# Kernel tuning notes

Measured on AMD Instinct MI355X. Metric: run time of the kernel, lower is better.

The kernel has to match this reference:

```python
import jax, jax.numpy as jnp
import numpy as np

RADIUS = 0.1
NSAMPLE = 32
B, N, NPOINT, C = 4, 8192, 2048, 64


def ball_query(xyz, new_xyz, fps_idx):
    """Faithful to pointnet2 ball_query CUDA kernel: for each centroid collect up to
    NSAMPLE in-radius point indices in scan order; slots beyond the count are padded
    with the first in-radius index (0 if the ball is empty). fps_idx is prepended."""
    n = xyz.shape[1]
    # squared distances (B, npoint, N)
    d2 = jnp.sum((new_xyz[:, :, None, :] - xyz[:, None, :, :]) ** 2, axis=-1)
    valid = d2 < jnp.float32(RADIUS) ** 2
    cand = jnp.where(valid, jnp.arange(n, dtype=jnp.int32), jnp.int32(n))
    cand = jnp.sort(cand, axis=-1)[:, :, :NSAMPLE]  # first NSAMPLE valid ids, N = sentinel
    first = cand[:, :, :1]
    pad = jnp.where(first < n, first, 0)            # pad with first valid (0 if none)
    idx = jnp.where(cand < n, cand, pad)
    return jnp.concatenate([fps_idx[:, :, None], idx], axis=2)  # (B, npoint, NSAMPLE+1)


def group(features, idx):
    # features (B, C, N), idx (B, npoint, K) -> (B, C, npoint, K)
    return jax.vmap(lambda f, i: f[:, i])(features, idx)


def setup_inputs() -> dict:
    key = jax.random.key(0)
    k1, k2, k3 = jax.random.split(key, 3)
    xyz = jax.random.uniform(k1, (B, N, 3), dtype=jnp.float32)
    fps_idx = jax.random.randint(k2, (B, NPOINT), 0, N, dtype=jnp.int32)
    new_xyz = jax.vmap(lambda p, i: p[i])(xyz, fps_idx)  # centroids are real points
    features = jax.random.normal(k3, (B, C, N), dtype=jnp.float32)
    return {"xyz": xyz, "new_xyz": new_xyz, "features": features, "fps_idx": fps_idx}


def reference(xyz, new_xyz, features, fps_idx):
    idx = jax.lax.stop_gradient(ball_query(xyz, new_xyz, fps_idx))
    grouped_xyz = group(jnp.swapaxes(xyz, 1, 2), idx)              # (B, 3, npoint, K)
    centered = grouped_xyz - jnp.swapaxes(new_xyz, 1, 2)[..., None]
    # NOTE: the torch module uses in-place `grouped_xyz -= ...`, so raw_grouped_xyz
    # aliases the centered tensor -> both concat slots hold centered coordinates.
    grouped_features = group(features, idx)                        # (B, C, npoint, K)
    return jnp.concatenate([centered, centered, grouped_features], axis=1)
```

## Files before the change

kernel.cpp:

```cpp
#include <hip/hip_runtime.h>
#include <stdint.h>
#include <limits.h>

constexpr int BB      = 4;
constexpr int NN      = 8192;
constexpr int NPOINT  = 2048;
constexpr int CC      = 64;
constexpr int NSAMPLE = 32;
constexpr int KTOT    = NSAMPLE + 1;
constexpr int NCH     = 3 + 3 + CC;
constexpr int CHS     = NPOINT * KTOT;

constexpr int   GG     = 5;
constexpr int   NCELL  = GG * GG * GG;
constexpr float RPADF  = 0.1001f;
constexpr int   CAND_CAP = 192;

__device__ __forceinline__ int cell_of(float x, float y, float z) {
    int ix = (int)floorf(x * 5.0f); ix = ix < 0 ? 0 : (ix > 4 ? 4 : ix);
    int iy = (int)floorf(y * 5.0f); iy = iy < 0 ? 0 : (iy > 4 ? 4 : iy);
    int iz = (int)floorf(z * 5.0f); iz = iz < 0 ? 0 : (iz > 4 ? 4 : iz);
    return (ix * GG + iy) * GG + iz;
}

__global__ __launch_bounds__(1024) void grid_build(
    const float* __restrict__ xyz, int* __restrict__ cellstartg,
    float4* __restrict__ spt)
{
    __shared__ int hist[NCELL];
    __shared__ int csl[NCELL + 1];
    __shared__ int cur[NCELL];
    const int b = blockIdx.x;
    const int t = threadIdx.x;
    if (t < NCELL) hist[t] = 0;
    __syncthreads();
    const float* xb = xyz + (size_t)b * NN * 3;
    float px[NN / 1024], py[NN / 1024], pz[NN / 1024];
    int   pc[NN / 1024];
#pragma unroll
    for (int k = 0; k < NN / 1024; ++k) {
        const float* p = xb + (size_t)(t + k * 1024) * 3;
        px[k] = p[0]; py[k] = p[1]; pz[k] = p[2];
        pc[k] = cell_of(px[k], py[k], pz[k]);
        atomicAdd(&hist[pc[k]], 1);
    }
    __syncthreads();
    if (t < 64) {
        int x0 = hist[t];
        int x1 = (t + 64 < NCELL) ? hist[t + 64] : 0;
#pragma unroll
        for (int d = 1; d < 64; d <<= 1) {
            int t0 = __shfl_up(x0, d);
            int t1 = __shfl_up(x1, d);
            if (t >= d) { x0 += t0; x1 += t1; }
        }
        x1 += __shfl(x0, 63);
        if (t == 0) csl[0] = 0;
        csl[1 + t] = x0;
        if (t <= 60) csl[65 + t] = x1;
    }
    __syncthreads();
    if (t < NCELL + 1) cellstartg[b * (NCELL + 1) + t] = csl[t];
    if (t < NCELL)     cur[t] = csl[t];
    __syncthreads();
#pragma unroll
    for (int k = 0; k < NN / 1024; ++k) {
        const int pos = atomicAdd(&cur[pc[k]], 1);
        spt[b * NN + pos] = make_float4(px[k], py[k], pz[k],
                                        __int_as_float(t + k * 1024));
    }
}

__global__ __launch_bounds__(256) void ball_query_grid(
    const float4* __restrict__ spt, const int* __restrict__ cellstart,
    const float* __restrict__ new_xyz, const int* __restrict__ fps_idx,
    int*         __restrict__ idx_out)
{
    __shared__ int cand[4][CAND_CAP];
    const int w    = threadIdx.x >> 6;
    const int lane = threadIdx.x & 63;
    const int wave = blockIdx.x * 4 + w;
    const int b    = wave >> 11;

    const float* cp = new_xyz + (size_t)wave * 3;
    const float cx = cp[0], cy = cp[1], cz = cp[2];
    const float r2 = __fmul_rn(0.1f, 0.1f);

    int ix0 = (int)floorf((cx - RPADF) * 5.0f); ix0 = ix0 < 0 ? 0 : ix0;
    int ix1 = (int)floorf((cx + RPADF) * 5.0f); ix1 = ix1 > 4 ? 4 : ix1;
    int iy0 = (int)floorf((cy - RPADF) * 5.0f); iy0 = iy0 < 0 ? 0 : iy0;
    int iy1 = (int)floorf((cy + RPADF) * 5.0f); iy1 = iy1 > 4 ? 4 : iy1;
    int iz0 = (int)floorf((cz - RPADF) * 5.0f); iz0 = iz0 < 0 ? 0 : iz0;
    int iz1 = (int)floorf((cz + RPADF) * 5.0f); iz1 = iz1 > 4 ? 4 : iz1;

    const int* cs = cellstart + b * (NCELL + 1);
    const int gb  = b * NN;
    int cnt = 0;

    for (int ix = ix0; ix <= ix1; ++ix) {
        for (int iy = iy0; iy <= iy1; ++iy) {
            const int cbase = (ix * GG + iy) * GG;
            const int st = cs[cbase + iz0];
            const int en = cs[cbase + iz1 + 1];
            for (int base = st; base < en; base += 64) {
                const int pos = base + lane;
                const bool inb = pos < en;
                const float4 q = spt[gb + (inb ? pos : st)];
                const int oid = __float_as_int(q.w);
                const float dx = __fsub_rn(cx, q.x);
                const float dy = __fsub_rn(cy, q.y);
                const float dz = __fsub_rn(cz, q.z);
                const float d2 = __fadd_rn(__fadd_rn(__fmul_rn(dx, dx), __fmul_rn(dy, dy)),
                                           __fmul_rn(dz, dz));
                const bool valid = inb && (d2 < r2);
                const unsigned long long m = __ballot(valid);
                if (m != 0ull) {
                    const int prefix = __builtin_amdgcn_mbcnt_hi(
                        (unsigned)(m >> 32), __builtin_amdgcn_mbcnt_lo((unsigned)m, 0u));
                    const int slot = cnt + prefix;
                    if (valid && slot < CAND_CAP) cand[w][slot] = oid;
                    cnt += (int)__popcll(m);
                }
            }
        }
    }

    const int K = cnt > CAND_CAP ? CAND_CAP : cnt;

    int v0 = (lane       < K) ? cand[w][lane]       : INT_MAX;
    int v1 = (lane + 64  < K) ? cand[w][lane + 64]  : INT_MAX;
    int v2 = (lane + 128 < K) ? cand[w][lane + 128] : INT_MAX;
    int rk0 = 0, rk1 = 0, rk2 = 0;
    for (int j = 0; j < K; ++j) {
        const int sv = cand[w][j];
        rk0 += (sv < v0); rk1 += (sv < v1); rk2 += (sv < v2);
    }
    int* out = idx_out + (size_t)wave * KTOT;
    if (lane       < K && rk0 < NSAMPLE) out[1 + rk0] = v0;
    if (lane + 64  < K && rk1 < NSAMPLE) out[1 + rk1] = v1;
    if (lane + 128 < K && rk2 < NSAMPLE) out[1 + rk2] = v2;

    if (K < NSAMPLE) {
        int mn = v0;
#pragma unroll
        for (int off = 32; off >= 1; off >>= 1) {
            const int o = __shfl_xor(mn, off);
            mn = o < mn ? o : mn;
        }
        const int pad = (K > 0) ? mn : 0;
        if (lane >= K && lane < NSAMPLE) out[1 + lane] = pad;
    }
    if (lane == 0) out[0] = fps_idx[wave];
}

__global__ __launch_bounds__(256) void feat_transpose(
    const float* __restrict__ f, float* __restrict__ ft)
{
    __shared__ float tile[64 * 65];
    const int blk = blockIdx.x;
    const int b   = blk >> 7;
    const int n0  = (blk & 127) << 6;
    const int w   = threadIdx.x >> 6, l = threadIdx.x & 63;
#pragma unroll
    for (int i = 0; i < 16; ++i) {
        const int c = i * 4 + w;
        tile[l * 65 + c] = f[((size_t)b * CC + c) * NN + n0 + l];
    }
    __syncthreads();
#pragma unroll
    for (int i = 0; i < 16; ++i) {
        const int flat = i * 256 + threadIdx.x;
        ft[((size_t)b * NN + n0) * CC + flat] = tile[(flat >> 6) * 65 + (flat & 63)];
    }
}

constexpr int TPAD = 66;
__global__ __launch_bounds__(256) void gather_v7(
    const float* __restrict__ xyz, const float* __restrict__ new_xyz,
    const float4* __restrict__ ft4, const int* __restrict__ idx,
    float* __restrict__ out)
{
    __shared__ float tile[NCH][TPAD];
    const int blk = blockIdx.x;
    const int t   = threadIdx.x;
    const int jj0 = blk * 64;
    const int b   = jj0 / CHS;
    const int jjb = jj0 - b * CHS;

    if (t < 64) {
        const int id = idx[jj0 + t];
        const int j  = (jjb + t) / KTOT;
        const float* gp = xyz + (size_t)(b * NN + id) * 3;
        const float* cp = new_xyz + (size_t)(b * NPOINT + j) * 3;
        const float vx = __fsub_rn(gp[0], cp[0]);
        const float vy = __fsub_rn(gp[1], cp[1]);
        const float vz = __fsub_rn(gp[2], cp[2]);
        tile[0][t] = vx; tile[1][t] = vy; tile[2][t] = vz;
        tile[3][t] = vx; tile[4][t] = vy; tile[5][t] = vz;
    }

    {
        const int r = t >> 2, g = t & 3;
        const int id = idx[jj0 + r];
        const float4* row = ft4 + ((size_t)b * NN + id) * (CC / 4);
        float4 v[4];
#pragma unroll
        for (int i = 0; i < 4; ++i) v[i] = row[4 * i + g];
#pragma unroll
        for (int i = 0; i < 4; ++i) {
            const int c0 = 6 + 16 * i + 4 * g;
            tile[c0 + 0][r] = v[i].x;
            tile[c0 + 1][r] = v[i].y;
            tile[c0 + 2][r] = v[i].z;
            tile[c0 + 3][r] = v[i].w;
        }
    }
    __syncthreads();

    const int w   = t >> 6;
    const int col = t & 63;
    const size_t ob = (size_t)b * NCH * CHS + (size_t)jjb + col;
#pragma unroll
    for (int k = 0; k < 18; ++k) {
        const int ch = 4 * k + w;
        if (ch < NCH) out[ob + (size_t)ch * CHS] = tile[ch][col];
    }
}

__global__ __launch_bounds__(256) void ball_query_bf(
    const float* __restrict__ xyz, const float* __restrict__ new_xyz,
    const int* __restrict__ fps_idx, int* __restrict__ idx_out)
{
    const int wave = (blockIdx.x * blockDim.x + threadIdx.x) >> 6;
    const int lane = threadIdx.x & 63;
    if (wave >= BB * NPOINT) return;
    const int b = wave >> 11;
    const float* cp = new_xyz + (size_t)wave * 3;
    const float cx = cp[0], cy = cp[1], cz = cp[2];
    const float r2 = __fmul_rn(0.1f, 0.1f);
    const float* xb = xyz + (size_t)b * NN * 3;
    int* out = idx_out + (size_t)wave * KTOT;
    int count = 0, first = 0;
    for (int base = 0; base < NN; base += 64) {
        const int p = base + lane;
        const float dx = __fsub_rn(cx, xb[p * 3 + 0]);
        const float dy = __fsub_rn(cy, xb[p * 3 + 1]);
        const float dz = __fsub_rn(cz, xb[p * 3 + 2]);
        const float d2 = __fadd_rn(__fadd_rn(__fmul_rn(dx, dx), __fmul_rn(dy, dy)),
                                   __fmul_rn(dz, dz));
        const bool valid = d2 < r2;
        const unsigned long long m = __ballot(valid);
        if (count == 0 && m != 0ull) first = base + __builtin_ctzll(m);
        const int prefix = __builtin_amdgcn_mbcnt_hi(
            (unsigned)(m >> 32), __builtin_amdgcn_mbcnt_lo((unsigned)m, 0u));
        const int slot = count + prefix;
        if (valid && slot < NSAMPLE) out[1 + slot] = p;
        count += (int)__popcll(m);
        if (count >= NSAMPLE) break;
    }
    if (count < NSAMPLE) {
        const int pad = (count > 0) ? first : 0;
        if (lane >= count && lane < NSAMPLE) out[1 + lane] = pad;
    }
    if (lane == 0) out[0] = fps_idx[wave];
}

__global__ __launch_bounds__(256) void gather_kernel(
    const float* __restrict__ xyz, const float* __restrict__ new_xyz,
    const float* __restrict__ features, const int* __restrict__ idx,
    float* __restrict__ out)
{
    const long long total = (long long)BB * NCH * CHS;
    const long long o = (long long)blockIdx.x * blockDim.x + threadIdx.x;
    if (o >= total) return;
    const int s  = (int)(o % KTOT);
    long long t  = o / KTOT;
    const int j  = (int)(t % NPOINT);
    t /= NPOINT;
    const int ch = (int)(t % NCH);
    const int b  = (int)(t / NCH);
    const int id = idx[(long long)(b * NPOINT + j) * KTOT + s];
    float v;
    if (ch < 6) {
        const int c3 = (ch >= 3) ? (ch - 3) : ch;
        v = __fsub_rn(xyz[((long long)b * NN + id) * 3 + c3],
                      new_xyz[((long long)b * NPOINT + j) * 3 + c3]);
    } else {
        v = features[((long long)b * CC + (ch - 6)) * NN + id];
    }
    out[o] = v;
}

extern "C" void kernel_launch(void* const* d_in, const int* in_sizes, int n_in,
                              void* d_out, int out_size, void* d_ws, size_t ws_size,
                              hipStream_t stream) {
    const float* xyz      = (const float*)d_in[0];
    const float* new_xyz  = (const float*)d_in[1];
    const float* features = (const float*)d_in[2];
    const int*   fps_idx  = (const int*)d_in[3];
    float*       out      = (float*)d_out;

    const size_t off_idx  = 0;
    const size_t sz_idx   = (size_t)BB * CHS * 4;
    const size_t off_ft   = off_idx + sz_idx;
    const size_t sz_ft    = (size_t)BB * NN * CC * 4;
    const size_t off_spt  = off_ft + sz_ft;
    const size_t sz_spt   = (size_t)BB * NN * 16;
    const size_t off_cs   = off_spt + sz_spt;
    const size_t need_full = off_cs + 2048;

    int* idxbuf = (int*)((char*)d_ws + off_idx);

    if (ws_size >= need_full) {
        float*  ft  = (float*) ((char*)d_ws + off_ft);
        float4* spt = (float4*)((char*)d_ws + off_spt);
        int*    cs  = (int*)   ((char*)d_ws + off_cs);

        grid_build<<<BB, 1024, 0, stream>>>(xyz, cs, spt);

        ball_query_grid<<<BB * NPOINT / 4, 256, 0, stream>>>(
            spt, cs, new_xyz, fps_idx, idxbuf);

        feat_transpose<<<BB * (NN / 64), 256, 0, stream>>>(features, ft);
        gather_v7<<<BB * CHS / 64, 256, 0, stream>>>(xyz, new_xyz, (const float4*)ft,
                                                     idxbuf, out);
    } else if (ws_size >= sz_idx) {
        ball_query_bf<<<BB * NPOINT / 4, 256, 0, stream>>>(xyz, new_xyz, fps_idx, idxbuf);
        const long long total = (long long)BB * NCH * CHS;
        gather_kernel<<<(int)((total + 255) / 256), 256, 0, stream>>>(
            xyz, new_xyz, features, idxbuf, out);
    }
}
```

Before: 124.1 us.

## Sort centroids by grid cell for locality and unroll ball-query scan by two

Result: no change. 126.5 us (+1.9%).

```diff
diff --git a/kernel.cpp b/kernel.cpp
--- a/kernel.cpp
+++ b/kernel.cpp
@@ -24,14 +24,16 @@
 }
 
 __global__ __launch_bounds__(1024) void grid_build(
-    const float* __restrict__ xyz, int* __restrict__ cellstartg,
-    float4* __restrict__ spt)
+    const float* __restrict__ xyz, const float* __restrict__ new_xyz,
+    int* __restrict__ cellstartg, float4* __restrict__ spt,
+    int* __restrict__ csortg)
 {
     __shared__ int hist[NCELL];
     __shared__ int csl[NCELL + 1];
     __shared__ int cur[NCELL];
     const int b = blockIdx.x;
     const int t = threadIdx.x;
+
     if (t < NCELL) hist[t] = 0;
     __syncthreads();
     const float* xb = xyz + (size_t)b * NN * 3;
@@ -69,20 +71,57 @@
         spt[b * NN + pos] = make_float4(px[k], py[k], pz[k],
                                         __int_as_float(t + k * 1024));
     }
+
+    __syncthreads();
+    if (t < NCELL) hist[t] = 0;
+    __syncthreads();
+    const float* nb = new_xyz + (size_t)b * NPOINT * 3;
+    int cc[NPOINT / 1024];
+#pragma unroll
+    for (int k = 0; k < NPOINT / 1024; ++k) {
+        const float* p = nb + (size_t)(t + k * 1024) * 3;
+        cc[k] = cell_of(p[0], p[1], p[2]);
+        atomicAdd(&hist[cc[k]], 1);
+    }
+    __syncthreads();
+    if (t < 64) {
+        int x0 = hist[t];
+        int x1 = (t + 64 < NCELL) ? hist[t + 64] : 0;
+#pragma unroll
+        for (int d = 1; d < 64; d <<= 1) {
+            int t0 = __shfl_up(x0, d);
+            int t1 = __shfl_up(x1, d);
+            if (t >= d) { x0 += t0; x1 += t1; }
+        }
+        x1 += __shfl(x0, 63);
+        if (t == 0) csl[0] = 0;
+        csl[1 + t] = x0;
+        if (t <= 60) csl[65 + t] = x1;
+    }
+    __syncthreads();
+    if (t < NCELL) cur[t] = csl[t];
+    __syncthreads();
+#pragma unroll
+    for (int k = 0; k < NPOINT / 1024; ++k) {
+        const int pos = atomicAdd(&cur[cc[k]], 1);
+        csortg[b * NPOINT + pos] = t + k * 1024;
+    }
 }
 
 __global__ __launch_bounds__(256) void ball_query_grid(
     const float4* __restrict__ spt, const int* __restrict__ cellstart,
+    const int* __restrict__ csort,
     const float* __restrict__ new_xyz, const int* __restrict__ fps_idx,
     int*         __restrict__ idx_out)
 {
     __shared__ int cand[4][CAND_CAP];
     const int w    = threadIdx.x >> 6;
     const int lane = threadIdx.x & 63;
-    const int wave = blockIdx.x * 4 + w;
-    const int b    = wave >> 11;
-
-    const float* cp = new_xyz + (size_t)wave * 3;
+    const int sp   = blockIdx.x * 4 + w;
+    const int b    = sp >> 11;
+    const int gc   = b * NPOINT + csort[sp];
+
+    const float* cp = new_xyz + (size_t)gc * 3;
     const float cx = cp[0], cy = cp[1], cz = cp[2];
     const float r2 = __fmul_rn(0.1f, 0.1f);
 
@@ -102,24 +141,44 @@
             const int cbase = (ix * GG + iy) * GG;
             const int st = cs[cbase + iz0];
             const int en = cs[cbase + iz1 + 1];
-            for (int base = st; base < en; base += 64) {
-                const int pos = base + lane;
-                const bool inb = pos < en;
-                const float4 q = spt[gb + (inb ? pos : st)];
-                const int oid = __float_as_int(q.w);
-                const float dx = __fsub_rn(cx, q.x);
-                const float dy = __fsub_rn(cy, q.y);
-                const float dz = __fsub_rn(cz, q.z);
-                const float d2 = __fadd_rn(__fadd_rn(__fmul_rn(dx, dx), __fmul_rn(dy, dy)),
-                                           __fmul_rn(dz, dz));
-                const bool valid = inb && (d2 < r2);
-                const unsigned long long m = __ballot(valid);
-                if (m != 0ull) {
-                    const int prefix = __builtin_amdgcn_mbcnt_hi(
-                        (unsigned)(m >> 32), __builtin_amdgcn_mbcnt_lo((unsigned)m, 0u));
-                    const int slot = cnt + prefix;
-                    if (valid && slot < CAND_CAP) cand[w][slot] = oid;
-                    cnt += (int)__popcll(m);
+            for (int base = st; base < en; base += 128) {
+                const int p0 = base + lane;
+                const int p1 = base + 64 + lane;
+                const bool i0 = p0 < en;
+                const bool i1 = p1 < en;
+                const float4 q0 = spt[gb + (i0 ? p0 : st)];
+                const float4 q1 = spt[gb + (i1 ? p1 : st)];
+                {
+                    const float dx = __fsub_rn(cx, q0.x);
+                    const float dy = __fsub_rn(cy, q0.y);
+                    const float dz = __fsub_rn(cz, q0.z);
+                    const float d2 = __fadd_rn(__fadd_rn(__fmul_rn(dx, dx), __fmul_rn(dy, dy)),
+                                               __fmul_rn(dz, dz));
+                    const bool valid = i0 && (d2 < r2);
+                    const unsigned long long m = __ballot(valid);
+                    if (m != 0ull) {
+                        const int prefix = __builtin_amdgcn_mbcnt_hi(
+                            (unsigned)(m >> 32), __builtin_amdgcn_mbcnt_lo((unsigned)m, 0u));
+                        const int slot = cnt + prefix;
+                        if (valid && slot < CAND_CAP) cand[w][slot] = __float_as_int(q0.w);
+                        cnt += (int)__popcll(m);
+                    }
+                }
+                {
+                    const float dx = __fsub_rn(cx, q1.x);
+                    const float dy = __fsub_rn(cy, q1.y);
+                    const float dz = __fsub_rn(cz, q1.z);
+                    const float d2 = __fadd_rn(__fadd_rn(__fmul_rn(dx, dx), __fmul_rn(dy, dy)),
+                                               __fmul_rn(dz, dz));
+                    const bool valid = i1 && (d2 < r2);
+                    const unsigned long long m = __ballot(valid);
+                    if (m != 0ull) {
+                        const int prefix = __builtin_amdgcn_mbcnt_hi(
+                            (unsigned)(m >> 32), __builtin_amdgcn_mbcnt_lo((unsigned)m, 0u));
+                        const int slot = cnt + prefix;
+                        if (valid && slot < CAND_CAP) cand[w][slot] = __float_as_int(q1.w);
+                        cnt += (int)__popcll(m);
+                    }
                 }
             }
         }
@@ -135,7 +194,7 @@
         const int sv = cand[w][j];
         rk0 += (sv < v0); rk1 += (sv < v1); rk2 += (sv < v2);
     }
-    int* out = idx_out + (size_t)wave * KTOT;
+    int* out = idx_out + (size_t)gc * KTOT;
     if (lane       < K && rk0 < NSAMPLE) out[1 + rk0] = v0;
     if (lane + 64  < K && rk1 < NSAMPLE) out[1 + rk1] = v1;
     if (lane + 128 < K && rk2 < NSAMPLE) out[1 + rk2] = v2;
@@ -150,7 +209,7 @@
         const int pad = (K > 0) ? mn : 0;
         if (lane >= K && lane < NSAMPLE) out[1 + lane] = pad;
     }
-    if (lane == 0) out[0] = fps_idx[wave];
+    if (lane == 0) out[0] = fps_idx[gc];
 }
 
 __global__ __launch_bounds__(256) void feat_transpose(
@@ -307,19 +366,22 @@
     const size_t off_spt  = off_ft + sz_ft;
     const size_t sz_spt   = (size_t)BB * NN * 16;
     const size_t off_cs   = off_spt + sz_spt;
-    const size_t need_full = off_cs + 2048;
+    const size_t off_csort = off_cs + 2048;
+    const size_t sz_csort  = (size_t)BB * NPOINT * 4;
+    const size_t need_full = off_csort + sz_csort;
 
     int* idxbuf = (int*)((char*)d_ws + off_idx);
 
     if (ws_size >= need_full) {
-        float*  ft  = (float*) ((char*)d_ws + off_ft);
-        float4* spt = (float4*)((char*)d_ws + off_spt);
-        int*    cs  = (int*)   ((char*)d_ws + off_cs);
-
-        grid_build<<<BB, 1024, 0, stream>>>(xyz, cs, spt);
+        float*  ft    = (float*) ((char*)d_ws + off_ft);
+        float4* spt   = (float4*)((char*)d_ws + off_spt);
+        int*    cs    = (int*)   ((char*)d_ws + off_cs);
+        int*    csort = (int*)   ((char*)d_ws + off_csort);
+
+        grid_build<<<BB, 1024, 0, stream>>>(xyz, new_xyz, cs, spt, csort);
 
         ball_query_grid<<<BB * NPOINT / 4, 256, 0, stream>>>(
-            spt, cs, new_xyz, fps_idx, idxbuf);
+            spt, cs, csort, new_xyz, fps_idx, idxbuf);
 
         feat_transpose<<<BB * (NN / 64), 256, 0, stream>>>(features, ft);
         gather_v7<<<BB * CHS / 64, 256, 0, stream>>>(xyz, new_xyz, (const float4*)ft,
```

## Fuse grid build with feature transpose and vectorize gather output stores

Applied to the files above, without the earlier changes.

Result: no change. 124.5 us (+0.3%).

```diff
diff --git a/kernel.cpp b/kernel.cpp
--- a/kernel.cpp
+++ b/kernel.cpp
@@ -23,51 +23,77 @@
     return (ix * GG + iy) * GG + iz;
 }
 
-__global__ __launch_bounds__(1024) void grid_build(
-    const float* __restrict__ xyz, int* __restrict__ cellstartg,
-    float4* __restrict__ spt)
-{
-    __shared__ int hist[NCELL];
-    __shared__ int csl[NCELL + 1];
-    __shared__ int cur[NCELL];
-    const int b = blockIdx.x;
-    const int t = threadIdx.x;
-    if (t < NCELL) hist[t] = 0;
-    __syncthreads();
-    const float* xb = xyz + (size_t)b * NN * 3;
-    float px[NN / 1024], py[NN / 1024], pz[NN / 1024];
-    int   pc[NN / 1024];
-#pragma unroll
-    for (int k = 0; k < NN / 1024; ++k) {
-        const float* p = xb + (size_t)(t + k * 1024) * 3;
-        px[k] = p[0]; py[k] = p[1]; pz[k] = p[2];
-        pc[k] = cell_of(px[k], py[k], pz[k]);
-        atomicAdd(&hist[pc[k]], 1);
-    }
-    __syncthreads();
-    if (t < 64) {
-        int x0 = hist[t];
-        int x1 = (t + 64 < NCELL) ? hist[t + 64] : 0;
-#pragma unroll
-        for (int d = 1; d < 64; d <<= 1) {
-            int t0 = __shfl_up(x0, d);
-            int t1 = __shfl_up(x1, d);
-            if (t >= d) { x0 += t0; x1 += t1; }
-        }
-        x1 += __shfl(x0, 63);
-        if (t == 0) csl[0] = 0;
-        csl[1 + t] = x0;
-        if (t <= 60) csl[65 + t] = x1;
-    }
-    __syncthreads();
-    if (t < NCELL + 1) cellstartg[b * (NCELL + 1) + t] = csl[t];
-    if (t < NCELL)     cur[t] = csl[t];
-    __syncthreads();
-#pragma unroll
-    for (int k = 0; k < NN / 1024; ++k) {
-        const int pos = atomicAdd(&cur[pc[k]], 1);
-        spt[b * NN + pos] = make_float4(px[k], py[k], pz[k],
-                                        __int_as_float(t + k * 1024));
+constexpr int TR_FLOATS = 256 * 65;
+__global__ __launch_bounds__(1024) void build_and_transpose(
+    const float* __restrict__ xyz, const float* __restrict__ features,
+    int* __restrict__ cellstartg, float4* __restrict__ spt,
+    float* __restrict__ ft)
+{
+    __shared__ float smem[TR_FLOATS];
+    const int blk = blockIdx.x;
+    const int t   = threadIdx.x;
+
+    if (blk < BB) {
+        int* hist = (int*)smem;
+        int* csl  = hist + NCELL;
+        int* cur  = csl + NCELL + 1;
+        const int b = blk;
+        if (t < NCELL) hist[t] = 0;
+        __syncthreads();
+        const float* xb = xyz + (size_t)b * NN * 3;
+        float px[NN / 1024], py[NN / 1024], pz[NN / 1024];
+        int   pc[NN / 1024];
+#pragma unroll
+        for (int k = 0; k < NN / 1024; ++k) {
+            const float* p = xb + (size_t)(t + k * 1024) * 3;
+            px[k] = p[0]; py[k] = p[1]; pz[k] = p[2];
+            pc[k] = cell_of(px[k], py[k], pz[k]);
+            atomicAdd(&hist[pc[k]], 1);
+        }
+        __syncthreads();
+        if (t < 64) {
+            int x0 = hist[t];
+            int x1 = (t + 64 < NCELL) ? hist[t + 64] : 0;
+#pragma unroll
+            for (int d = 1; d < 64; d <<= 1) {
+                int t0 = __shfl_up(x0, d);
+                int t1 = __shfl_up(x1, d);
+                if (t >= d) { x0 += t0; x1 += t1; }
+            }
+            x1 += __shfl(x0, 63);
+            if (t == 0) csl[0] = 0;
+            csl[1 + t] = x0;
+            if (t <= 60) csl[65 + t] = x1;
+        }
+        __syncthreads();
+        if (t < NCELL + 1) cellstartg[b * (NCELL + 1) + t] = csl[t];
+        if (t < NCELL)     cur[t] = csl[t];
+        __syncthreads();
+#pragma unroll
+        for (int k = 0; k < NN / 1024; ++k) {
+            const int pos = atomicAdd(&cur[pc[k]], 1);
+            spt[b * NN + pos] = make_float4(px[k], py[k], pz[k],
+                                            __int_as_float(t + k * 1024));
+        }
+    } else {
+        const int bt  = blk - BB;
+        const int b   = bt >> 5;
+        const int n0  = (bt & 31) << 8;
+#pragma unroll
+        for (int i = 0; i < 16; ++i) {
+            const int flat = i * 1024 + t;
+            const int c = flat >> 8;
+            const int j = flat & 255;
+            smem[j * 65 + c] = features[((size_t)b * CC + c) * NN + n0 + j];
+        }
+        __syncthreads();
+#pragma unroll
+        for (int i = 0; i < 16; ++i) {
+            const int flat = i * 1024 + t;
+            const int n = flat >> 6;
+            const int c = flat & 63;
+            ft[((size_t)b * NN + n0 + n) * CC + c] = smem[n * 65 + c];
+        }
     }
 }
 
@@ -153,29 +179,8 @@
     if (lane == 0) out[0] = fps_idx[wave];
 }
 
-__global__ __launch_bounds__(256) void feat_transpose(
-    const float* __restrict__ f, float* __restrict__ ft)
-{
-    __shared__ float tile[64 * 65];
-    const int blk = blockIdx.x;
-    const int b   = blk >> 7;
-    const int n0  = (blk & 127) << 6;
-    const int w   = threadIdx.x >> 6, l = threadIdx.x & 63;
-#pragma unroll
-    for (int i = 0; i < 16; ++i) {
-        const int c = i * 4 + w;
-        tile[l * 65 + c] = f[((size_t)b * CC + c) * NN + n0 + l];
-    }
-    __syncthreads();
-#pragma unroll
-    for (int i = 0; i < 16; ++i) {
-        const int flat = i * 256 + threadIdx.x;
-        ft[((size_t)b * NN + n0) * CC + flat] = tile[(flat >> 6) * 65 + (flat & 63)];
-    }
-}
-
-constexpr int TPAD = 66;
-__global__ __launch_bounds__(256) void gather_v7(
+constexpr int TPAD = 68;
+__global__ __launch_bounds__(256) void gather_v8(
     const float* __restrict__ xyz, const float* __restrict__ new_xyz,
     const float4* __restrict__ ft4, const int* __restrict__ idx,
     float* __restrict__ out)
@@ -217,13 +222,16 @@
     }
     __syncthreads();
 
-    const int w   = t >> 6;
-    const int col = t & 63;
-    const size_t ob = (size_t)b * NCH * CHS + (size_t)jjb + col;
-#pragma unroll
-    for (int k = 0; k < 18; ++k) {
-        const int ch = 4 * k + w;
-        if (ch < NCH) out[ob + (size_t)ch * CHS] = tile[ch][col];
+    const size_t outb = (size_t)b * NCH * CHS + (size_t)jjb;
+#pragma unroll
+    for (int m = 0; m < 5; ++m) {
+        const int fidx = m * 256 + t;
+        if (fidx < NCH * 16) {
+            const int ch = fidx >> 4;
+            const int fc = fidx & 15;
+            const float4 v = *(const float4*)&tile[ch][fc * 4];
+            *(float4*)(out + outb + (size_t)ch * CHS + 4 * fc) = v;
+        }
     }
 }
 
@@ -316,14 +324,14 @@
         float4* spt = (float4*)((char*)d_ws + off_spt);
         int*    cs  = (int*)   ((char*)d_ws + off_cs);
 
-        grid_build<<<BB, 1024, 0, stream>>>(xyz, cs, spt);
+        build_and_transpose<<<BB + 128, 1024, 0, stream>>>(
+            xyz, features, cs, spt, ft);
 
         ball_query_grid<<<BB * NPOINT / 4, 256, 0, stream>>>(
             spt, cs, new_xyz, fps_idx, idxbuf);
 
-        feat_transpose<<<BB * (NN / 64), 256, 0, stream>>>(features, ft);
-        gather_v7<<<BB * CHS / 64, 256, 0, stream>>>(xyz, new_xyz, (const float4*)ft,
-                                                     idxbuf, out);
+        gather_v8<<<BB * CHS / 64, 256, 0, stream>>>(
+            xyz, new_xyz, (const float4*)ft, idxbuf, out);
     } else if (ws_size >= sz_idx) {
         ball_query_bf<<<BB * NPOINT / 4, 256, 0, stream>>>(xyz, new_xyz, fps_idx, idxbuf);
         const long long total = (long long)BB * NCH * CHS;
```
